# Optimization experiments

Measured on AMD Instinct MI355X. Metric: run time of the kernel, lower is better.

The kernel has to match this reference:

```python
import jax, jax.numpy as jnp
import numpy as np
from jax import lax

B, T, I, H = 64, 512, 256, 512  # batch, time, input_size, hidden_size
HH = H // 2


def setup_inputs() -> dict:
    key = jax.random.key(0)
    ks = jax.random.split(key, 6)
    input_tensor = jax.random.normal(ks[0], (B, T, I), dtype=jnp.float32)
    memories = jax.random.normal(ks[1], (1, B, HH + 2 * H), dtype=jnp.float32)
    # torch LSTM params, gate order (i, f, g, o); forget_bias=1.0 added to f-block of bias
    W_ih = jax.random.normal(ks[2], (4 * H, I), dtype=jnp.float32) * (1.0 / np.sqrt(I))
    W_hh = jax.random.normal(ks[3], (4 * H, H), dtype=jnp.float32) * (1.0 / np.sqrt(H))
    b_ih = jnp.zeros((4 * H,), dtype=jnp.float32).at[H:2 * H].set(1.0)  # forget bias
    b_hh = jnp.zeros((4 * H,), dtype=jnp.float32)
    return {"input_tensor": input_tensor, "memories": memories,
            "W_ih": W_ih, "W_hh": W_hh, "b_ih": b_ih, "b_hh": b_hh}


@jax.custom_vjp
def ptmax(a, b):
    return jnp.maximum(a, b)

def _ptmax_fwd(a, b):
    return jnp.maximum(a, b), None

def _ptmax_bwd(_, g):
    # straight-through: gradient passes to BOTH inputs
    return (g, g)

ptmax.defvjp(_ptmax_fwd, _ptmax_bwd)


def reference(input_tensor, memories, W_ih, W_hh, b_ih, b_hh):
    # split memories: acc [1,B,HH], h0/c0 [B,H]
    acc = memories[..., :HH][0]          # [B, HH] (torch m is [B,1,HH])
    h0 = memories[..., HH:HH + H][0]     # [B, H]
    c0 = memories[..., HH + H:][0]       # [B, H]

    bias = b_ih + b_hh                   # [4H]
    xs = jnp.swapaxes(input_tensor, 0, 1)  # [T, B, I] time-major

    def lstm_step(carry, x_t):
        h, c = carry
        gates = x_t @ W_ih.T + h @ W_hh.T + bias  # [B, 4H]
        i, f, g, o = jnp.split(gates, 4, axis=-1)
        c = jax.nn.sigmoid(f) * c + jax.nn.sigmoid(i) * jnp.tanh(g)
        h = jax.nn.sigmoid(o) * jnpp_tanh(c) if False else jax.nn.sigmoid(o) * jnp.tanh(c)
        return (h, c), h

    (hT, cT), hs = lax.scan(lstm_step, (h0, c0), xs)  # hs: [T, B, H]

    h_half = hs[..., :HH]   # [T, B, HH]
    other = hs[..., HH:]    # [T, B, HH]

    def max_step(m, h_t):
        m2 = ptmax(m, h_t)
        return m2, m2

    m_final, cmax = lax.scan(max_step, acc, h_half)  # cmax: [T, B, HH]

    concat_out = jnp.swapaxes(jnp.concatenate([cmax, other], axis=-1), 0, 1)  # [B, T, H]
    output_mem = jnp.concatenate([m_final[None], hT[None], cT[None]], axis=-1)  # [1, B, HH+2H]
    return concat_out, output_mem
```

## Files before the change

### kernel.cpp

```cpp
#include <hip/hip_runtime.h>
#include <stdint.h>

#define TT 512
#define BB 64
#define II 256
#define HS 512
#define HHALF 256
#define R4H 2048
#define HB_STRIDE 16384

typedef __attribute__((ext_vector_type(8))) short short8v;
typedef __attribute__((ext_vector_type(4))) float f32x4;

__global__ __launch_bounds__(256) void pregemm(
    const float* __restrict__ X,
    const float* __restrict__ Wih,
    const float* __restrict__ bih,
    const float* __restrict__ bhh,
    float* __restrict__ PG)
{
  __shared__ __align__(16) float Xs[64][68];
  __shared__ __align__(16) float Ws[64][68];
  const int t = blockIdx.x;
  const int rbase = blockIdx.y * 64;
  const int tid = threadIdx.x;
  const int cg = tid & 15;
  const int rg = tid >> 4;

  float acc[4][4] = {};

  for (int k0 = 0; k0 < II; k0 += 64) {
    {
      int b = tid >> 2, kq = tid & 3;
      const float* src = X + ((size_t)b * TT + t) * II + k0 + kq * 16;
      #pragma unroll
      for (int i = 0; i < 16; i += 4) {
        float4 v = *(const float4*)(src + i);
        int kk = kq * 16 + i;
        Xs[kk + 0][b] = v.x; Xs[kk + 1][b] = v.y;
        Xs[kk + 2][b] = v.z; Xs[kk + 3][b] = v.w;
      }
    }
    {
      int r = tid >> 2, kq = tid & 3;
      const float* src = Wih + (size_t)(rbase + r) * II + k0 + kq * 16;
      #pragma unroll
      for (int i = 0; i < 16; i += 4) {
        float4 v = *(const float4*)(src + i);
        int kk = kq * 16 + i;
        Ws[kk + 0][r] = v.x; Ws[kk + 1][r] = v.y;
        Ws[kk + 2][r] = v.z; Ws[kk + 3][r] = v.w;
      }
    }
    __syncthreads();
    #pragma unroll 8
    for (int kk = 0; kk < 64; ++kk) {
      float4 a = *(const float4*)&Ws[kk][rg * 4];
      float4 x = *(const float4*)&Xs[kk][cg * 4];
      float av[4] = {a.x, a.y, a.z, a.w};
      float xv[4] = {x.x, x.y, x.z, x.w};
      #pragma unroll
      for (int i = 0; i < 4; ++i)
        #pragma unroll
        for (int j = 0; j < 4; ++j)
          acc[i][j] = fmaf(av[i], xv[j], acc[i][j]);
    }
    __syncthreads();
  }

  #pragma unroll
  for (int i = 0; i < 4; ++i) {
    int row = rbase + rg * 4 + i;
    float bias = bih[row] + bhh[row];
    float4 o;
    o.x = acc[i][0] + bias; o.y = acc[i][1] + bias;
    o.z = acc[i][2] + bias; o.w = acc[i][3] + bias;
    *(float4*)&PG[((size_t)t * R4H + row) * BB + cg * 4] = o;
  }
}

__device__ __forceinline__ uint32_t bf16r(float f) {
  uint32_t u = __float_as_uint(f);
  u += 0x7fffu + ((u >> 16) & 1u);
  return u >> 16;
}

__global__ void init_h(const float* __restrict__ mem, uint32_t* __restrict__ hb)
{
  int idx = blockIdx.x * 256 + threadIdx.x;
  if (idx < HB_STRIDE) {
    int uh = idx >> 6, b = idx & 63;
    float lo = mem[(size_t)b * 1280 + 256 + 2 * uh];
    float hi = mem[(size_t)b * 1280 + 256 + 2 * uh + 1];
    hb[idx] = bf16r(lo) | (bf16r(hi) << 16);
  }
}

__device__ __forceinline__ void store_coh_u32(uint32_t* p, uint32_t v) {
  (void)__hip_atomic_exchange(p, v, __ATOMIC_RELAXED, __HIP_MEMORY_SCOPE_AGENT);
}
__device__ __forceinline__ uint32_t load_coh_u32(const uint32_t* p) {
  return __hip_atomic_load(p, __ATOMIC_RELAXED, __HIP_MEMORY_SCOPE_AGENT);
}

#define GIDX(row, col) (((row) << 6) + ((col) ^ ((((row) >> 2) & 1) << 4)))

__global__ __launch_bounds__(512) void lstm_persistent(
    const float* __restrict__ mem,
    const float* __restrict__ Whh,
    float* __restrict__ PG,
    uint32_t* __restrict__ hb,
    float* __restrict__ outmem,
    unsigned* __restrict__ bar)
{
  extern __shared__ uint32_t smem[];
  uint32_t* WA = smem;
  uint32_t* HL = smem + 8192;
  float*  gsum = (float*)(smem + 8192 + 16896);

  const int g    = blockIdx.x;
  const int tid  = threadIdx.x;
  const int wu   = tid >> 6;
  const int lane = tid & 63;
  const int l15  = lane & 15;
  const int lq   = lane >> 4;
  const int bt   = wu & 3;
  const int rt   = wu >> 2;
  const int u0   = g * 8;

  unsigned* cnt = bar;
  unsigned* gen = bar + 64;

  #pragma unroll
  for (int s = 0; s < 4; ++s) {
    int slot = s * 512 + tid;
    int srt  = slot >> 10;
    int rem  = slot & 1023;
    int sks  = rem >> 6;
    int ln   = rem & 63;
    int sl15 = ln & 15, slq = ln >> 4;
    int lr   = srt * 16 + sl15;
    int grow = (lr >> 3) * HS + u0 + (lr & 7);
    const float* wp = Whh + (size_t)grow * HS + slq * 8 + sks * 32;
    float4 x0 = *(const float4*)(wp);
    float4 x1 = *(const float4*)(wp + 4);
    uint32_t* dst = WA + (size_t)slot * 4;
    dst[0] = bf16r(x0.x) | (bf16r(x0.y) << 16);
    dst[1] = bf16r(x0.z) | (bf16r(x0.w) << 16);
    dst[2] = bf16r(x1.x) | (bf16r(x1.y) << 16);
    dst[3] = bf16r(x1.z) | (bf16r(x1.w) << 16);
  }

  const int p = tid >> 6;
  const int eb = lane;
  float c0 = 0.f, c1 = 0.f, m0 = 0.f, m1 = 0.f, h0l = 0.f, h1l = 0.f;
  if (tid < 256) {
    c0 = mem[(size_t)eb * 1280 + 768 + u0 + 2 * p];
    c1 = mem[(size_t)eb * 1280 + 768 + u0 + 2 * p + 1];
    if (u0 < HHALF) {
      m0 = mem[(size_t)eb * 1280 + u0 + 2 * p];
      m1 = mem[(size_t)eb * 1280 + u0 + 2 * p + 1];
    }
  }

  float pg[4];
  #pragma unroll
  for (int r = 0; r < 4; ++r) {
    int lr = rt * 16 + lq * 4 + r;
    pg[r] = PG[((size_t)0 * R4H + (lr >> 3) * HS + u0 + (lr & 7)) * BB + bt * 16 + l15];
  }

  __syncthreads();

  const uint32_t* waBase = WA + ((size_t)(rt * 16) * 64 + lane) * 4;
  const int hlCol = bt * 16 + l15;

  for (int t = 0; t < TT; ++t) {
    {
      const uint32_t* hcur = hb + (size_t)(t & 1) * HB_STRIDE;
      uint32_t hv[32];
      #pragma unroll
      for (int i = 0; i < 32; ++i) hv[i] = load_coh_u32(hcur + tid + i * 512);
      #pragma unroll
      for (int i = 0; i < 32; ++i) {
        int w = tid + i * 512;
        HL[(w >> 6) * 66 + (w & 63)] = hv[i];
      }
    }
    __syncthreads();

    f32x4 acc = {0.f, 0.f, 0.f, 0.f};
    #pragma unroll
    for (int ks = 0; ks < 16; ++ks) {
      short8v av = *(const short8v*)(waBase + ks * 256);
      union { uint32_t u[4]; short8v v; } bf;
      #pragma unroll
      for (int m = 0; m < 4; ++m)
        bf.u[m] = HL[(ks * 16 + lq * 4 + m) * 66 + hlCol];
      acc = __builtin_amdgcn_mfma_f32_16x16x32_bf16(av, bf.v, acc, 0, 0, 0);
    }

    {
      const int colw = bt * 16 + l15;
      #pragma unroll
      for (int r = 0; r < 4; ++r) {
        int row = rt * 16 + lq * 4 + r;
        gsum[GIDX(row, colw)] = acc[r] + pg[r];
      }
    }
    __syncthreads();

    if (tid < 256) {
      const int ul0 = 2 * p, ul1 = 2 * p + 1;
      float gi0 = gsum[GIDX( 0 + ul0, eb)];
      float gf0 = gsum[GIDX( 8 + ul0, eb)];
      float gg0 = gsum[GIDX(16 + ul0, eb)];
      float go0 = gsum[GIDX(24 + ul0, eb)];
      float gi1 = gsum[GIDX( 0 + ul1, eb)];
      float gf1 = gsum[GIDX( 8 + ul1, eb)];
      float gg1 = gsum[GIDX(16 + ul1, eb)];
      float go1 = gsum[GIDX(24 + ul1, eb)];
      float si0 = 1.f / (1.f + __expf(-gi0));
      float sf0 = 1.f / (1.f + __expf(-gf0));
      float so0 = 1.f / (1.f + __expf(-go0));
      float si1 = 1.f / (1.f + __expf(-gi1));
      float sf1 = 1.f / (1.f + __expf(-gf1));
      float so1 = 1.f / (1.f + __expf(-go1));
      c0 = sf0 * c0 + si0 * tanhf(gg0);
      c1 = sf1 * c1 + si1 * tanhf(gg1);
      float h0 = so0 * tanhf(c0);
      float h1 = so1 * tanhf(c1);
      h0l = h0; h1l = h1;
      store_coh_u32(&hb[(size_t)((t + 1) & 1) * HB_STRIDE + (size_t)(g * 4 + p) * 64 + eb],
                    bf16r(h0) | (bf16r(h1) << 16));
      float out0 = h0, out1 = h1;
      if (u0 < HHALF) { m0 = fmaxf(m0, h0); m1 = fmaxf(m1, h1); out0 = m0; out1 = m1; }
      PG[((size_t)t * R4H + u0 + 2 * p) * BB + eb]     = out0;
      PG[((size_t)t * R4H + u0 + 2 * p + 1) * BB + eb] = out1;
    }

    asm volatile("s_waitcnt vmcnt(0)" ::: "memory");
    __syncthreads();
    if (t + 1 < TT) {
      #pragma unroll
      for (int r = 0; r < 4; ++r) {
        int lr = rt * 16 + lq * 4 + r;
        pg[r] = PG[((size_t)(t + 1) * R4H + (lr >> 3) * HS + u0 + (lr & 7)) * BB + bt * 16 + l15];
      }
    }
    if (tid == 0) {
      unsigned a = __hip_atomic_fetch_add(cnt, 1u, __ATOMIC_RELAXED,
                                          __HIP_MEMORY_SCOPE_AGENT);
      if (a == 64u * (unsigned)(t + 1) - 1u)
        (void)__hip_atomic_exchange(gen, (unsigned)(t + 1), __ATOMIC_RELAXED,
                                    __HIP_MEMORY_SCOPE_AGENT);
      int spins = 0;
      while (__hip_atomic_load(gen, __ATOMIC_RELAXED,
                               __HIP_MEMORY_SCOPE_AGENT) < (unsigned)(t + 1)) {
        __builtin_amdgcn_s_sleep(1);
        if (++spins > (1 << 16)) break;
      }
    }
    __syncthreads();
  }

  if (tid < 256) {
    outmem[(size_t)eb * 1280 + 256 + u0 + 2 * p]     = h0l;
    outmem[(size_t)eb * 1280 + 256 + u0 + 2 * p + 1] = h1l;
    outmem[(size_t)eb * 1280 + 768 + u0 + 2 * p]     = c0;
    outmem[(size_t)eb * 1280 + 768 + u0 + 2 * p + 1] = c1;
    if (u0 < HHALF) {
      outmem[(size_t)eb * 1280 + u0 + 2 * p]     = m0;
      outmem[(size_t)eb * 1280 + u0 + 2 * p + 1] = m1;
    }
  }
}

__global__ __launch_bounds__(256) void transpose_out(
    const float* __restrict__ PG, float* __restrict__ out)
{
  __shared__ __align__(16) float tileS[64][68];
  const int t = blockIdx.x;
  const int u0 = blockIdx.y * 64;
  const int tid = threadIdx.x;

  {
    int cg = tid & 15, rg = tid >> 4;
    const float* src = PG + (size_t)t * R4H * BB + (size_t)u0 * BB;
    #pragma unroll
    for (int i = 0; i < 4; ++i) {
      int u = rg * 4 + i;
      float4 v = *(const float4*)(src + (size_t)u * BB + cg * 4);
      *(float4*)&tileS[u][cg * 4] = v;
    }
  }
  __syncthreads();
  {
    int ug = tid & 15, bg = tid >> 4;
    #pragma unroll
    for (int i = 0; i < 4; ++i) {
      int b = bg * 4 + i;
      float4 o;
      o.x = tileS[ug * 4 + 0][b];
      o.y = tileS[ug * 4 + 1][b];
      o.z = tileS[ug * 4 + 2][b];
      o.w = tileS[ug * 4 + 3][b];
      *(float4*)&out[((size_t)b * TT + t) * HS + u0 + ug * 4] = o;
    }
  }
}

extern "C" void kernel_launch(void* const* d_in, const int* in_sizes, int n_in,
                              void* d_out, int out_size, void* d_ws, size_t ws_size,
                              hipStream_t stream)
{
  const float* X   = (const float*)d_in[0];
  const float* mem = (const float*)d_in[1];
  const float* Wih = (const float*)d_in[2];
  const float* Whh = (const float*)d_in[3];
  const float* bih = (const float*)d_in[4];
  const float* bhh = (const float*)d_in[5];

  float* out = (float*)d_out;
  float* outmem = out + (size_t)BB * TT * HS;

  float* PG     = (float*)d_ws;
  uint32_t* hbp = (uint32_t*)(PG + (size_t)TT * R4H * BB);
  unsigned* bar = (unsigned*)(hbp + 2 * HB_STRIDE);

  const int dyn_lds = 108544;
  (void)hipFuncSetAttribute((const void*)lstm_persistent,
                            hipFuncAttributeMaxDynamicSharedMemorySize, dyn_lds);

  hipMemsetAsync(bar, 0, 2048 * sizeof(unsigned), stream);
  init_h<<<dim3(HB_STRIDE / 256), dim3(256), 0, stream>>>(mem, hbp);
  pregemm<<<dim3(TT, 32), dim3(256), 0, stream>>>(X, Wih, bih, bhh, PG);
  lstm_persistent<<<dim3(64), dim3(512), dyn_lds, stream>>>(mem, Whh, PG, hbp, outmem, bar);
  transpose_out<<<dim3(TT, 8), dim3(256), 0, stream>>>(PG, out);
}
```

Before: 3.023 ms.

## Fuse input GEMM and output transpose into the persistent LSTM kernel

Replaces the separate pregemm, recurrent and transpose kernels with one 256-block persistent kernel. Blocks 0-63 run the recurrence, and the other 192 blocks first compute the input-projection tiles and then transpose finished timesteps to the output. Producer and consumer blocks hand off through per-timestep completion counters and the existing generation barrier. This is meant to hide the input GEMM and the transpose behind the serial recurrence and to remove launch gaps. In exchange, it relies on all 256 blocks being co-resident, adds flag spinning to the critical path, and may add memory contention from the helper blocks.

```diff
diff --git a/kernel.cpp b/kernel.cpp
--- a/kernel.cpp
+++ b/kernel.cpp
@@ -11,73 +11,6 @@
 
 typedef __attribute__((ext_vector_type(8))) short short8v;
 typedef __attribute__((ext_vector_type(4))) float f32x4;
-
-__global__ __launch_bounds__(256) void pregemm(
-    const float* __restrict__ X,
-    const float* __restrict__ Wih,
-    const float* __restrict__ bih,
-    const float* __restrict__ bhh,
-    float* __restrict__ PG)
-{
-  __shared__ __align__(16) float Xs[64][68];
-  __shared__ __align__(16) float Ws[64][68];
-  const int t = blockIdx.x;
-  const int rbase = blockIdx.y * 64;
-  const int tid = threadIdx.x;
-  const int cg = tid & 15;
-  const int rg = tid >> 4;
-
-  float acc[4][4] = {};
-
-  for (int k0 = 0; k0 < II; k0 += 64) {
-    {
-      int b = tid >> 2, kq = tid & 3;
-      const float* src = X + ((size_t)b * TT + t) * II + k0 + kq * 16;
-      #pragma unroll
-      for (int i = 0; i < 16; i += 4) {
-        float4 v = *(const float4*)(src + i);
-        int kk = kq * 16 + i;
-        Xs[kk + 0][b] = v.x; Xs[kk + 1][b] = v.y;
-        Xs[kk + 2][b] = v.z; Xs[kk + 3][b] = v.w;
-      }
-    }
-    {
-      int r = tid >> 2, kq = tid & 3;
-      const float* src = Wih + (size_t)(rbase + r) * II + k0 + kq * 16;
-      #pragma unroll
-      for (int i = 0; i < 16; i += 4) {
-        float4 v = *(const float4*)(src + i);
-        int kk = kq * 16 + i;
-        Ws[kk + 0][r] = v.x; Ws[kk + 1][r] = v.y;
-        Ws[kk + 2][r] = v.z; Ws[kk + 3][r] = v.w;
-      }
-    }
-    __syncthreads();
-    #pragma unroll 8
-    for (int kk = 0; kk < 64; ++kk) {
-      float4 a = *(const float4*)&Ws[kk][rg * 4];
-      float4 x = *(const float4*)&Xs[kk][cg * 4];
-      float av[4] = {a.x, a.y, a.z, a.w};
-      float xv[4] = {x.x, x.y, x.z, x.w};
-      #pragma unroll
-      for (int i = 0; i < 4; ++i)
-        #pragma unroll
-        for (int j = 0; j < 4; ++j)
-          acc[i][j] = fmaf(av[i], xv[j], acc[i][j]);
-    }
-    __syncthreads();
-  }
-
-  #pragma unroll
-  for (int i = 0; i < 4; ++i) {
-    int row = rbase + rg * 4 + i;
-    float bias = bih[row] + bhh[row];
-    float4 o;
-    o.x = acc[i][0] + bias; o.y = acc[i][1] + bias;
-    o.z = acc[i][2] + bias; o.w = acc[i][3] + bias;
-    *(float4*)&PG[((size_t)t * R4H + row) * BB + cg * 4] = o;
-  }
-}
 
 __device__ __forceinline__ uint32_t bf16r(float f) {
   uint32_t u = __float_as_uint(f);
@@ -102,210 +35,308 @@
 __device__ __forceinline__ uint32_t load_coh_u32(const uint32_t* p) {
   return __hip_atomic_load(p, __ATOMIC_RELAXED, __HIP_MEMORY_SCOPE_AGENT);
 }
+__device__ __forceinline__ void store_coh_f32(float* p, float v) {
+  store_coh_u32((uint32_t*)p, __float_as_uint(v));
+}
+__device__ __forceinline__ float load_coh_f32(const float* p) {
+  return __uint_as_float(load_coh_u32((const uint32_t*)p));
+}
 
 #define GIDX(row, col) (((row) << 6) + ((col) ^ ((((row) >> 2) & 1) << 4)))
 
-__global__ __launch_bounds__(512) void lstm_persistent(
+__global__ __launch_bounds__(512) void fused_lstm(
     const float* __restrict__ mem,
     const float* __restrict__ Whh,
+    const float* __restrict__ X,
+    const float* __restrict__ Wih,
+    const float* __restrict__ bih,
+    const float* __restrict__ bhh,
     float* __restrict__ PG,
     uint32_t* __restrict__ hb,
+    float* __restrict__ out,
     float* __restrict__ outmem,
     unsigned* __restrict__ bar)
 {
   extern __shared__ uint32_t smem[];
-  uint32_t* WA = smem;
-  uint32_t* HL = smem + 8192;
-  float*  gsum = (float*)(smem + 8192 + 16896);
-
-  const int g    = blockIdx.x;
-  const int tid  = threadIdx.x;
-  const int wu   = tid >> 6;
-  const int lane = tid & 63;
-  const int l15  = lane & 15;
-  const int lq   = lane >> 4;
-  const int bt   = wu & 3;
-  const int rt   = wu >> 2;
-  const int u0   = g * 8;
-
-  unsigned* cnt = bar;
-  unsigned* gen = bar + 64;
-
-  #pragma unroll
-  for (int s = 0; s < 4; ++s) {
-    int slot = s * 512 + tid;
-    int srt  = slot >> 10;
-    int rem  = slot & 1023;
-    int sks  = rem >> 6;
-    int ln   = rem & 63;
-    int sl15 = ln & 15, slq = ln >> 4;
-    int lr   = srt * 16 + sl15;
-    int grow = (lr >> 3) * HS + u0 + (lr & 7);
-    const float* wp = Whh + (size_t)grow * HS + slq * 8 + sks * 32;
-    float4 x0 = *(const float4*)(wp);
-    float4 x1 = *(const float4*)(wp + 4);
-    uint32_t* dst = WA + (size_t)slot * 4;
-    dst[0] = bf16r(x0.x) | (bf16r(x0.y) << 16);
-    dst[1] = bf16r(x0.z) | (bf16r(x0.w) << 16);
-    dst[2] = bf16r(x1.x) | (bf16r(x1.y) << 16);
-    dst[3] = bf16r(x1.z) | (bf16r(x1.w) << 16);
-  }
-
-  const int p = tid >> 6;
-  const int eb = lane;
-  float c0 = 0.f, c1 = 0.f, m0 = 0.f, m1 = 0.f, h0l = 0.f, h1l = 0.f;
-  if (tid < 256) {
-    c0 = mem[(size_t)eb * 1280 + 768 + u0 + 2 * p];
-    c1 = mem[(size_t)eb * 1280 + 768 + u0 + 2 * p + 1];
-    if (u0 < HHALF) {
-      m0 = mem[(size_t)eb * 1280 + u0 + 2 * p];
-      m1 = mem[(size_t)eb * 1280 + u0 + 2 * p + 1];
-    }
-  }
-
-  float pg[4];
-  #pragma unroll
-  for (int r = 0; r < 4; ++r) {
-    int lr = rt * 16 + lq * 4 + r;
-    pg[r] = PG[((size_t)0 * R4H + (lr >> 3) * HS + u0 + (lr & 7)) * BB + bt * 16 + l15];
-  }
-
-  __syncthreads();
-
-  const uint32_t* waBase = WA + ((size_t)(rt * 16) * 64 + lane) * 4;
-  const int hlCol = bt * 16 + l15;
-
-  for (int t = 0; t < TT; ++t) {
-    {
-      const uint32_t* hcur = hb + (size_t)(t & 1) * HB_STRIDE;
-      uint32_t hv[32];
-      #pragma unroll
-      for (int i = 0; i < 32; ++i) hv[i] = load_coh_u32(hcur + tid + i * 512);
-      #pragma unroll
-      for (int i = 0; i < 32; ++i) {
-        int w = tid + i * 512;
-        HL[(w >> 6) * 66 + (w & 63)] = hv[i];
+  const int g   = blockIdx.x;
+  const int tid = threadIdx.x;
+  unsigned* cnt    = bar;
+  unsigned* gen    = bar + 64;
+  unsigned* pgdone = bar + 128;
+
+  if (g < 64) {
+    uint32_t* WA = smem;
+    uint32_t* HL = smem + 8192;
+    float*  gsum = (float*)(smem + 8192 + 16896);
+
+    const int wu   = tid >> 6;
+    const int lane = tid & 63;
+    const int l15  = lane & 15;
+    const int lq   = lane >> 4;
+    const int bt   = wu & 3;
+    const int rt   = wu >> 2;
+    const int u0   = g * 8;
+
+    #pragma unroll
+    for (int s = 0; s < 4; ++s) {
+      int slot = s * 512 + tid;
+      int srt  = slot >> 10;
+      int rem  = slot & 1023;
+      int sks  = rem >> 6;
+      int ln   = rem & 63;
+      int sl15 = ln & 15, slq = ln >> 4;
+      int lr   = srt * 16 + sl15;
+      int grow = (lr >> 3) * HS + u0 + (lr & 7);
+      const float* wp = Whh + (size_t)grow * HS + slq * 8 + sks * 32;
+      float4 x0 = *(const float4*)(wp);
+      float4 x1 = *(const float4*)(wp + 4);
+      uint32_t* dst = WA + (size_t)slot * 4;
+      dst[0] = bf16r(x0.x) | (bf16r(x0.y) << 16);
+      dst[1] = bf16r(x0.z) | (bf16r(x0.w) << 16);
+      dst[2] = bf16r(x1.x) | (bf16r(x1.y) << 16);
+      dst[3] = bf16r(x1.z) | (bf16r(x1.w) << 16);
+    }
+
+    const int p = tid >> 6;
+    const int eb = lane;
+    float c0 = 0.f, c1 = 0.f, m0 = 0.f, m1 = 0.f, h0l = 0.f, h1l = 0.f;
+    if (tid < 256) {
+      c0 = mem[(size_t)eb * 1280 + 768 + u0 + 2 * p];
+      c1 = mem[(size_t)eb * 1280 + 768 + u0 + 2 * p + 1];
+      if (u0 < HHALF) {
+        m0 = mem[(size_t)eb * 1280 + u0 + 2 * p];
+        m1 = mem[(size_t)eb * 1280 + u0 + 2 * p + 1];
+      }
+    }
+
+    if (tid == 0) {
+      int spins = 0;
+      while (__hip_atomic_load(pgdone, __ATOMIC_RELAXED,
+                               __HIP_MEMORY_SCOPE_AGENT) < 32u) {
+        __builtin_amdgcn_s_sleep(2);
+        if (++spins > (1 << 17)) break;
       }
     }
     __syncthreads();
 
-    f32x4 acc = {0.f, 0.f, 0.f, 0.f};
-    #pragma unroll
-    for (int ks = 0; ks < 16; ++ks) {
-      short8v av = *(const short8v*)(waBase + ks * 256);
-      union { uint32_t u[4]; short8v v; } bf;
-      #pragma unroll
-      for (int m = 0; m < 4; ++m)
-        bf.u[m] = HL[(ks * 16 + lq * 4 + m) * 66 + hlCol];
-      acc = __builtin_amdgcn_mfma_f32_16x16x32_bf16(av, bf.v, acc, 0, 0, 0);
-    }
-
-    {
-      const int colw = bt * 16 + l15;
-      #pragma unroll
-      for (int r = 0; r < 4; ++r) {
-        int row = rt * 16 + lq * 4 + r;
-        gsum[GIDX(row, colw)] = acc[r] + pg[r];
-      }
-    }
-    __syncthreads();
-
-    if (tid < 256) {
-      const int ul0 = 2 * p, ul1 = 2 * p + 1;
-      float gi0 = gsum[GIDX( 0 + ul0, eb)];
-      float gf0 = gsum[GIDX( 8 + ul0, eb)];
-      float gg0 = gsum[GIDX(16 + ul0, eb)];
-      float go0 = gsum[GIDX(24 + ul0, eb)];
-      float gi1 = gsum[GIDX( 0 + ul1, eb)];
-      float gf1 = gsum[GIDX( 8 + ul1, eb)];
-      float gg1 = gsum[GIDX(16 + ul1, eb)];
-      float go1 = gsum[GIDX(24 + ul1, eb)];
-      float si0 = 1.f / (1.f + __expf(-gi0));
-      float sf0 = 1.f / (1.f + __expf(-gf0));
-      float so0 = 1.f / (1.f + __expf(-go0));
-      float si1 = 1.f / (1.f + __expf(-gi1));
-      float sf1 = 1.f / (1.f + __expf(-gf1));
-      float so1 = 1.f / (1.f + __expf(-go1));
-      c0 = sf0 * c0 + si0 * tanhf(gg0);
-      c1 = sf1 * c1 + si1 * tanhf(gg1);
-      float h0 = so0 * tanhf(c0);
-      float h1 = so1 * tanhf(c1);
-      h0l = h0; h1l = h1;
-      store_coh_u32(&hb[(size_t)((t + 1) & 1) * HB_STRIDE + (size_t)(g * 4 + p) * 64 + eb],
-                    bf16r(h0) | (bf16r(h1) << 16));
-      float out0 = h0, out1 = h1;
-      if (u0 < HHALF) { m0 = fmaxf(m0, h0); m1 = fmaxf(m1, h1); out0 = m0; out1 = m1; }
-      PG[((size_t)t * R4H + u0 + 2 * p) * BB + eb]     = out0;
-      PG[((size_t)t * R4H + u0 + 2 * p + 1) * BB + eb] = out1;
-    }
-
-    asm volatile("s_waitcnt vmcnt(0)" ::: "memory");
-    __syncthreads();
-    if (t + 1 < TT) {
+    const uint32_t* waBase = WA + ((size_t)(rt * 16) * 64 + lane) * 4;
+    const int hlCol = bt * 16 + l15;
+
+    for (int t = 0; t < TT; ++t) {
+      float pg[4];
       #pragma unroll
       for (int r = 0; r < 4; ++r) {
         int lr = rt * 16 + lq * 4 + r;
-        pg[r] = PG[((size_t)(t + 1) * R4H + (lr >> 3) * HS + u0 + (lr & 7)) * BB + bt * 16 + l15];
-      }
-    }
-    if (tid == 0) {
-      unsigned a = __hip_atomic_fetch_add(cnt, 1u, __ATOMIC_RELAXED,
-                                          __HIP_MEMORY_SCOPE_AGENT);
-      if (a == 64u * (unsigned)(t + 1) - 1u)
-        (void)__hip_atomic_exchange(gen, (unsigned)(t + 1), __ATOMIC_RELAXED,
-                                    __HIP_MEMORY_SCOPE_AGENT);
-      int spins = 0;
-      while (__hip_atomic_load(gen, __ATOMIC_RELAXED,
-                               __HIP_MEMORY_SCOPE_AGENT) < (unsigned)(t + 1)) {
-        __builtin_amdgcn_s_sleep(1);
-        if (++spins > (1 << 16)) break;
-      }
-    }
-    __syncthreads();
-  }
-
-  if (tid < 256) {
-    outmem[(size_t)eb * 1280 + 256 + u0 + 2 * p]     = h0l;
-    outmem[(size_t)eb * 1280 + 256 + u0 + 2 * p + 1] = h1l;
-    outmem[(size_t)eb * 1280 + 768 + u0 + 2 * p]     = c0;
-    outmem[(size_t)eb * 1280 + 768 + u0 + 2 * p + 1] = c1;
-    if (u0 < HHALF) {
-      outmem[(size_t)eb * 1280 + u0 + 2 * p]     = m0;
-      outmem[(size_t)eb * 1280 + u0 + 2 * p + 1] = m1;
-    }
-  }
-}
-
-__global__ __launch_bounds__(256) void transpose_out(
-    const float* __restrict__ PG, float* __restrict__ out)
-{
-  __shared__ __align__(16) float tileS[64][68];
-  const int t = blockIdx.x;
-  const int u0 = blockIdx.y * 64;
-  const int tid = threadIdx.x;
-
-  {
-    int cg = tid & 15, rg = tid >> 4;
-    const float* src = PG + (size_t)t * R4H * BB + (size_t)u0 * BB;
-    #pragma unroll
-    for (int i = 0; i < 4; ++i) {
-      int u = rg * 4 + i;
-      float4 v = *(const float4*)(src + (size_t)u * BB + cg * 4);
-      *(float4*)&tileS[u][cg * 4] = v;
-    }
-  }
-  __syncthreads();
-  {
-    int ug = tid & 15, bg = tid >> 4;
-    #pragma unroll
-    for (int i = 0; i < 4; ++i) {
-      int b = bg * 4 + i;
-      float4 o;
-      o.x = tileS[ug * 4 + 0][b];
-      o.y = tileS[ug * 4 + 1][b];
-      o.z = tileS[ug * 4 + 2][b];
-      o.w = tileS[ug * 4 + 3][b];
-      *(float4*)&out[((size_t)b * TT + t) * HS + u0 + ug * 4] = o;
+        pg[r] = load_coh_f32(&PG[((size_t)t * R4H + (lr >> 3) * HS + u0 + (lr & 7)) * BB + bt * 16 + l15]);
+      }
+
+      {
+        const uint32_t* hcur = hb + (size_t)(t & 1) * HB_STRIDE;
+        uint32_t hv[32];
+        #pragma unroll
+        for (int i = 0; i < 32; ++i) hv[i] = load_coh_u32(hcur + tid + i * 512);
+        #pragma unroll
+        for (int i = 0; i < 32; ++i) {
+          int w = tid + i * 512;
+          HL[(w >> 6) * 66 + (w & 63)] = hv[i];
+        }
+      }
+      __syncthreads();
+
+      f32x4 acc = {0.f, 0.f, 0.f, 0.f};
+      #pragma unroll
+      for (int ks = 0; ks < 16; ++ks) {
+        short8v av = *(const short8v*)(waBase + ks * 256);
+        union { uint32_t u[4]; short8v v; } bf;
+        #pragma unroll
+        for (int m = 0; m < 4; ++m)
+          bf.u[m] = HL[(ks * 16 + lq * 4 + m) * 66 + hlCol];
+        acc = __builtin_amdgcn_mfma_f32_16x16x32_bf16(av, bf.v, acc, 0, 0, 0);
+      }
+
+      {
+        const int colw = bt * 16 + l15;
+        #pragma unroll
+        for (int r = 0; r < 4; ++r) {
+          int row = rt * 16 + lq * 4 + r;
+          gsum[GIDX(row, colw)] = acc[r] + pg[r];
+        }
+      }
+      __syncthreads();
+
+      if (tid < 256) {
+        const int ul0 = 2 * p, ul1 = 2 * p + 1;
+        float gi0 = gsum[GIDX( 0 + ul0, eb)];
+        float gf0 = gsum[GIDX( 8 + ul0, eb)];
+        float gg0 = gsum[GIDX(16 + ul0, eb)];
+        float go0 = gsum[GIDX(24 + ul0, eb)];
+        float gi1 = gsum[GIDX( 0 + ul1, eb)];
+        float gf1 = gsum[GIDX( 8 + ul1, eb)];
+        float gg1 = gsum[GIDX(16 + ul1, eb)];
+        float go1 = gsum[GIDX(24 + ul1, eb)];
+        float si0 = 1.f / (1.f + __expf(-gi0));
+        float sf0 = 1.f / (1.f + __expf(-gf0));
+        float so0 = 1.f / (1.f + __expf(-go0));
+        float si1 = 1.f / (1.f + __expf(-gi1));
+        float sf1 = 1.f / (1.f + __expf(-gf1));
+        float so1 = 1.f / (1.f + __expf(-go1));
+        c0 = sf0 * c0 + si0 * tanhf(gg0);
+        c1 = sf1 * c1 + si1 * tanhf(gg1);
+        float h0 = so0 * tanhf(c0);
+        float h1 = so1 * tanhf(c1);
+        h0l = h0; h1l = h1;
+        store_coh_u32(&hb[(size_t)((t + 1) & 1) * HB_STRIDE + (size_t)(g * 4 + p) * 64 + eb],
+                      bf16r(h0) | (bf16r(h1) << 16));
+        float out0 = h0, out1 = h1;
+        if (u0 < HHALF) { m0 = fmaxf(m0, h0); m1 = fmaxf(m1, h1); out0 = m0; out1 = m1; }
+        store_coh_f32(&PG[((size_t)t * R4H + u0 + 2 * p) * BB + eb], out0);
+        store_coh_f32(&PG[((size_t)t * R4H + u0 + 2 * p + 1) * BB + eb], out1);
+      }
+
+      asm volatile("s_waitcnt vmcnt(0)" ::: "memory");
+      __syncthreads();
+      if (tid == 0) {
+        unsigned a = __hip_atomic_fetch_add(cnt, 1u, __ATOMIC_RELAXED,
+                                            __HIP_MEMORY_SCOPE_AGENT);
+        if (a == 64u * (unsigned)(t + 1) - 1u)
+          (void)__hip_atomic_exchange(gen, (unsigned)(t + 1), __ATOMIC_RELAXED,
+                                      __HIP_MEMORY_SCOPE_AGENT);
+        int spins = 0;
+        while (__hip_atomic_load(gen, __ATOMIC_RELAXED,
+                                 __HIP_MEMORY_SCOPE_AGENT) < (unsigned)(t + 1)) {
+          __builtin_amdgcn_s_sleep(1);
+          if (++spins > (1 << 16)) break;
+        }
+        if (t + 1 < TT) {
+          spins = 0;
+          while (__hip_atomic_load(pgdone + t + 1, __ATOMIC_RELAXED,
+                                   __HIP_MEMORY_SCOPE_AGENT) < 32u) {
+            __builtin_amdgcn_s_sleep(1);
+            if (++spins > (1 << 16)) break;
+          }
+        }
+      }
+      __syncthreads();
+    }
+
+    if (tid < 256) {
+      outmem[(size_t)eb * 1280 + 256 + u0 + 2 * p]     = h0l;
+      outmem[(size_t)eb * 1280 + 256 + u0 + 2 * p + 1] = h1l;
+      outmem[(size_t)eb * 1280 + 768 + u0 + 2 * p]     = c0;
+      outmem[(size_t)eb * 1280 + 768 + u0 + 2 * p + 1] = c1;
+      if (u0 < HHALF) {
+        outmem[(size_t)eb * 1280 + u0 + 2 * p]     = m0;
+        outmem[(size_t)eb * 1280 + u0 + 2 * p + 1] = m1;
+      }
+    }
+  } else {
+    const int hh = g - 64;
+    float* XsH  = (float*)smem;
+    float* Ws0H = XsH + 64 * 68;
+    float* Ws1H = Ws0H + 64 * 68;
+    float* LOut = Ws1H + 64 * 68;
+    uint32_t* TR = smem;
+
+    const int hf = tid >> 8;
+    const int t256 = tid & 255;
+    const int cg = t256 & 15, rg = t256 >> 4;
+
+    for (int tp = hh; tp < 8192; tp += 192) {
+      const int t = tp >> 4, rp = tp & 15;
+      float acc[4][4] = {};
+      for (int k0 = 0; k0 < II; k0 += 64) {
+        __syncthreads();
+        #pragma unroll
+        for (int ps = 0; ps < 6; ++ps) {
+          int slot = ps * 512 + tid;
+          int arr = slot >> 10;
+          int idx = slot & 1023;
+          int r = idx >> 4, q = idx & 15;
+          const float* src;
+          float* dst;
+          if (arr == 0) { src = X + ((size_t)r * TT + t) * II + k0 + q * 4; dst = XsH; }
+          else {
+            int rb = (rp * 2 + arr - 1) * 64;
+            src = Wih + (size_t)(rb + r) * II + k0 + q * 4;
+            dst = (arr == 1) ? Ws0H : Ws1H;
+          }
+          float4 v = *(const float4*)src;
+          dst[(q * 4 + 0) * 68 + r] = v.x;
+          dst[(q * 4 + 1) * 68 + r] = v.y;
+          dst[(q * 4 + 2) * 68 + r] = v.z;
+          dst[(q * 4 + 3) * 68 + r] = v.w;
+        }
+        __syncthreads();
+        const float* WsH = hf ? Ws1H : Ws0H;
+        #pragma unroll 8
+        for (int kk = 0; kk < 64; ++kk) {
+          float4 a = *(const float4*)&WsH[kk * 68 + rg * 4];
+          float4 x = *(const float4*)&XsH[kk * 68 + cg * 4];
+          float av[4] = {a.x, a.y, a.z, a.w};
+          float xv[4] = {x.x, x.y, x.z, x.w};
+          #pragma unroll
+          for (int i = 0; i < 4; ++i)
+            #pragma unroll
+            for (int j = 0; j < 4; ++j)
+              acc[i][j] = fmaf(av[i], xv[j], acc[i][j]);
+        }
+      }
+      {
+        int rbH = (rp * 2 + hf) * 64;
+        #pragma unroll
+        for (int i = 0; i < 4; ++i) {
+          int row = rg * 4 + i;
+          float bias = bih[rbH + row] + bhh[rbH + row];
+          #pragma unroll
+          for (int j = 0; j < 4; ++j)
+            LOut[hf * 4224 + row * 66 + cg * 4 + j] = acc[i][j] + bias;
+        }
+      }
+      __syncthreads();
+      {
+        uint32_t* pgU = (uint32_t*)PG + ((size_t)t * R4H + (rp * 2 + hf) * 64) * BB;
+        #pragma unroll
+        for (int j = 0; j < 16; ++j) {
+          int e = j * 256 + t256;
+          store_coh_u32(pgU + e,
+                        __float_as_uint(LOut[hf * 4224 + (e >> 6) * 66 + (e & 63)]));
+        }
+      }
+      asm volatile("s_waitcnt vmcnt(0)" ::: "memory");
+      __syncthreads();
+      if (tid == 0)
+        (void)__hip_atomic_fetch_add(pgdone + t, 2u, __ATOMIC_RELAXED,
+                                     __HIP_MEMORY_SCOPE_AGENT);
+    }
+
+    for (int ti = hh; ti < 4096; ti += 192) {
+      const int t = ti >> 3, ut = ti & 7;
+      if (tid == 0) {
+        int spins = 0;
+        while (__hip_atomic_load(gen, __ATOMIC_RELAXED,
+                                 __HIP_MEMORY_SCOPE_AGENT) < (unsigned)(t + 1)) {
+          __builtin_amdgcn_s_sleep(2);
+          if (++spins > (1 << 17)) break;
+        }
+      }
+      __syncthreads();
+      const uint32_t* srcU = (const uint32_t*)PG + ((size_t)t * R4H + ut * 64) * BB;
+      #pragma unroll
+      for (int j = 0; j < 8; ++j) {
+        int e = j * 512 + tid;
+        TR[(e >> 6) * 66 + (e & 63)] = load_coh_u32(srcU + e);
+      }
+      __syncthreads();
+      {
+        int w = tid >> 6, lane = tid & 63;
+        #pragma unroll
+        for (int bb = 0; bb < 8; ++bb) {
+          int b = w * 8 + bb;
+          out[((size_t)b * TT + t) * HS + ut * 64 + lane] =
+              __uint_as_float(TR[lane * 66 + b]);
+        }
+      }
+      __syncthreads();
     }
   }
 }
@@ -329,12 +360,11 @@
   unsigned* bar = (unsigned*)(hbp + 2 * HB_STRIDE);
 
   const int dyn_lds = 108544;
-  (void)hipFuncSetAttribute((const void*)lstm_persistent,
+  (void)hipFuncSetAttribute((const void*)fused_lstm,
                             hipFuncAttributeMaxDynamicSharedMemorySize, dyn_lds);
 
   hipMemsetAsync(bar, 0, 2048 * sizeof(unsigned), stream);
   init_h<<<dim3(HB_STRIDE / 256), dim3(256), 0, stream>>>(mem, hbp);
-  pregemm<<<dim3(TT, 32), dim3(256), 0, stream>>>(X, Wih, bih, bhh, PG);
-  lstm_persistent<<<dim3(64), dim3(512), dyn_lds, stream>>>(mem, Whh, PG, hbp, outmem, bar);
-  transpose_out<<<dim3(TT, 8), dim3(256), 0, stream>>>(PG, out);
-}
+  fused_lstm<<<dim3(256), dim3(512), dyn_lds, stream>>>(
+      mem, Whh, X, Wih, bih, bhh, PG, hbp, out, outmem, bar);
+}
```

Result: faster. 2.679 ms (-11.4%).
